# Optimization experiments

Hardware: AMD Instinct MI355X
Metric: run time of the kernel (lower is better)

## Reference

```python
import jax, jax.numpy as jnp
import numpy as np

B = 262144
N_DIM = 8
N_SPLIT = 4
DEPTH = 8
WIDTH = 32
ALPHA = 0.6
LOGSCALE_FACTOR = 3.0


def setup_inputs() -> dict:
    key = jax.random.key(0)
    ks = jax.random.split(key, 8)
    n_out = (N_DIM - N_SPLIT) * 2  # 8
    inp = {
        "x": jax.random.normal(ks[0], (B, N_DIM), dtype=jnp.float32),
        "logdet": jnp.zeros((B, 1), dtype=jnp.float32),
        # actnorm params (stacked over depth)
        "b": jnp.zeros((DEPTH, 1, N_DIM), dtype=jnp.float32),
        "logs": jnp.zeros((DEPTH, 1, N_DIM), dtype=jnp.float32),
        # affine coupling params
        "log_gamma": jnp.zeros((DEPTH, 1, N_DIM - N_SPLIT), dtype=jnp.float32),
        "W1": jax.random.normal(ks[1], (DEPTH, N_SPLIT, WIDTH), dtype=jnp.float32) / np.sqrt(N_SPLIT),
        "b1": jnp.zeros((DEPTH, WIDTH), dtype=jnp.float32),
        "W2": jax.random.normal(ks[2], (DEPTH, WIDTH, WIDTH), dtype=jnp.float32) / np.sqrt(WIDTH),
        "b2": jnp.zeros((DEPTH, WIDTH), dtype=jnp.float32),
        "Wf": jax.random.normal(ks[3], (DEPTH, WIDTH, n_out), dtype=jnp.float32) / np.sqrt(WIDTH),
        "bf": jnp.zeros((DEPTH, n_out), dtype=jnp.float32),
    }
    return inp


def _flow_forward(x, logdet, b, logs, log_gamma, W1, b1, W2, b2, Wf, bf):
    z = x
    ld = logdet
    for i in range(DEPTH):
        # ---- actnorm (with data-dependent init, detached as in torch) ----
        m = jnp.mean(z, axis=0, keepdims=True)
        v = jnp.mean(jnp.square(z - m), axis=0, keepdims=True)
        b_init = jax.lax.stop_gradient(-m)
        logs_init = jax.lax.stop_gradient(
            jnp.log(1.0 / (jnp.sqrt(v) + 1e-6)) / LOGSCALE_FACTOR)
        s = jnp.clip(logs[i] + logs_init, -5.0, 5.0)
        z = (z + (b[i] + b_init)) * jnp.exp(s)
        ld = ld + jnp.sum(s)
        # ---- affine coupling ----
        z1 = z[:, :N_SPLIT]
        z2 = z[:, N_SPLIT:]
        h = jax.nn.relu(z1 @ W1[i] + b1[i])
        h = jax.nn.relu(h @ W2[i] + b2[i])
        h = h @ Wf[i] + bf[i]                      # [B, 2*(n_dim-ns)]
        shift = h[:, 0::2]
        scale = ALPHA * jnp.tanh(h[:, 1::2])
        shift = jnp.exp(jnp.clip(log_gamma[i], -5.0, 5.0)) * jnp.tanh(shift)
        z2 = z2 + scale * z2 + shift
        ld = ld + jnp.sum(jnp.log1p(scale), axis=1, keepdims=True)
        z = jnp.concatenate([z1, z2], axis=1)
        # ---- flip ----
        z = z[:, ::-1]
    return z, ld


def reference(x, logdet, b, logs, log_gamma, W1, b1, W2, b2, Wf, bf):
    return _flow_forward(x, logdet, b, logs, log_gamma, W1, b1, W2, b2, Wf, bf)
```

## Files before the change

### kernel.cpp

```cpp
#include <hip/hip_runtime.h>

#define B_ROWS 262144
#define TPB 1024
#define NBLK 256
#define NGRP 64
#define PADW 32

#define SLOT_L_DW (16 * 64)
#define SLOTS_TOT (9 * SLOT_L_DW)
#define STATS_L_DW 32
#define STATS_TOT (9 * STATS_L_DW)

#define GF_OFF   (NGRP * PADW)
#define BAR_DWORDS (2 * NGRP * PADW)

typedef _Float16 f16;
typedef __attribute__((ext_vector_type(2))) __fp16 fp16x2_t;
typedef __attribute__((ext_vector_type(8))) _Float16 f16x8;
typedef __attribute__((ext_vector_type(4))) float f32x4;
typedef __attribute__((ext_vector_type(16))) float f32x16;
typedef __attribute__((ext_vector_type(2))) unsigned u32x2;

__device__ __forceinline__ float fast_tanh(float x) {
    float e = __expf(2.0f * x);
    return 1.0f - 2.0f * __builtin_amdgcn_rcpf(e + 1.0f);
}
__device__ __forceinline__ float pkh(float a, float b) {
    fp16x2_t h = __builtin_amdgcn_cvt_pkrtz(a, b);
    return __builtin_bit_cast(float, h);
}
__device__ __forceinline__ f16x8 mk8(float a, float b, float c, float d) {
    f32x4 v = {a, b, c, d};
    return __builtin_bit_cast(f16x8, v);
}
__device__ __forceinline__ float bcf(unsigned u) { return __builtin_bit_cast(float, u); }
__device__ __forceinline__ u32x2 pls(float a, float b) {
    return __builtin_amdgcn_permlane32_swap(
        __builtin_bit_cast(unsigned, a), __builtin_bit_cast(unsigned, b),
        false, false);
}

__device__ __forceinline__ void gbar_stats(
    float* slots, float* stats, unsigned* bar, unsigned target, int Lx,
    const float* logs, const float* bvec, const float* lgam, float* lred)
{
    const int tid  = threadIdx.x;
    const int lane = tid & 63;
    const int wid  = tid >> 6;
    const int bid  = blockIdx.x;
    __syncthreads();
    if (wid == 0) {
        if (lane == 0)
            __hip_atomic_fetch_add(bar + (bid >> 2) * PADW, 1u,
                                   __ATOMIC_ACQ_REL, __HIP_MEMORY_SCOPE_AGENT);
        if (bid == 0) {
            const unsigned t4 = target * (NBLK / NGRP);
            while (true) {
                unsigned c = __hip_atomic_load(bar + lane * PADW, __ATOMIC_RELAXED,
                                               __HIP_MEMORY_SCOPE_AGENT);
                if (__all(c >= t4)) break;
                __builtin_amdgcn_s_sleep(1);
            }
            __threadfence();
            const float* sl = slots + (size_t)Lx * SLOT_L_DW;
            float a16[16];
            #pragma unroll
            for (int j = 0; j < 16; ++j)
                a16[j] = __hip_atomic_load(sl + j * 64 + lane, __ATOMIC_RELAXED,
                                           __HIP_MEMORY_SCOPE_AGENT);
            #pragma unroll
            for (int d = 1; d < 64; d <<= 1) {
                #pragma unroll
                for (int j = 0; j < 16; ++j) a16[j] += __shfl_xor(a16[j], d, 64);
            }
            const float invB = 1.0f / (float)B_ROWS;
            float lv0 = 0.f, lv1 = 0.f, sl8 = 0.f, gf = 0.f;
            if (lane < 8) {
                float m = a16[lane] * invB;
                float q = a16[8 + lane] * invB;
                float v = q - m * m;
                v = v < 0.f ? 0.f : v;
                float li = -(1.0f / 3.0f) * __logf(sqrtf(v) + 1e-6f);
                float s = logs[Lx * 8 + lane] + li;
                s = s < -5.f ? -5.f : (s > 5.f ? 5.f : s);
                lv0 = __expf(s);
                lv1 = bvec[Lx * 8 + lane] - m;
                sl8 = s;
            } else if (lane < 12) {
                float lg = lgam[Lx * 4 + (lane - 8)];
                lg = lg < -5.f ? -5.f : (lg > 5.f ? 5.f : lg);
                gf = __expf(lg);
            }
            float ss = sl8;
            ss += __shfl_xor(ss, 1, 64);
            ss += __shfl_xor(ss, 2, 64);
            ss += __shfl_xor(ss, 4, 64);
            float* st = stats + (size_t)Lx * STATS_L_DW;
            if (lane < 8) {
                __hip_atomic_store(st + lane, lv0, __ATOMIC_RELAXED,
                                   __HIP_MEMORY_SCOPE_AGENT);
                __hip_atomic_store(st + 8 + lane, lv1, __ATOMIC_RELAXED,
                                   __HIP_MEMORY_SCOPE_AGENT);
                lred[lane] = lv0; lred[8 + lane] = lv1;
            } else if (lane < 12) {
                __hip_atomic_store(st + 8 + lane, gf, __ATOMIC_RELAXED,
                                   __HIP_MEMORY_SCOPE_AGENT);
                lred[8 + lane] = gf;
            }
            if (lane == 0) {
                __hip_atomic_store(st + 20, ss, __ATOMIC_RELAXED,
                                   __HIP_MEMORY_SCOPE_AGENT);
                lred[20] = ss;
            }
            __hip_atomic_store(bar + GF_OFF + lane * PADW, target,
                               __ATOMIC_RELEASE, __HIP_MEMORY_SCOPE_AGENT);
        } else {
            unsigned* gfp = bar + GF_OFF + (bid >> 2) * PADW;
            while (__hip_atomic_load(gfp, __ATOMIC_RELAXED,
                                     __HIP_MEMORY_SCOPE_AGENT) < target)
                __builtin_amdgcn_s_sleep(1);
            (void)__hip_atomic_load(gfp, __ATOMIC_ACQUIRE,
                                    __HIP_MEMORY_SCOPE_AGENT);
            if (lane < 21)
                lred[lane] = __hip_atomic_load(stats + (size_t)Lx * STATS_L_DW + lane,
                                               __ATOMIC_RELAXED,
                                               __HIP_MEMORY_SCOPE_AGENT);
        }
    }
    __syncthreads();
}

#define PKBLK 80
__global__ void __launch_bounds__(256)
pack_weights(const float* __restrict__ W1, const float* __restrict__ W2,
             const float* __restrict__ Wf,
             f16* __restrict__ w1pk, f16* __restrict__ w2pk, f16* __restrict__ wfpk,
             float* __restrict__ slots, unsigned* __restrict__ bar)
{
    int i = blockIdx.x * 256 + threadIdx.x;
    if (i < 16384) {
        int which = i >> 13;
        int t  = i & 8191;
        int j  = t & 7;
        int ln = (t >> 3) & 63;
        int kh = (t >> 9) & 1;
        int L  = t >> 10;
        int k  = kh * 16 + ((ln >> 5) << 3) + j;
        if (which == 0) {
            w2pk[t] = (f16)W2[L * 1024 + k * 32 + (ln & 31)];
        } else {
            int row = ln & 31;
            wfpk[t] = (row < 8) ? (f16)Wf[L * 256 + k * 8 + row] : (f16)0.f;
        }
    } else {
        int t  = i - 16384;
        int j  = t & 7;
        int ln = (t >> 3) & 63;
        int L  = t >> 9;
        int k  = ((ln >> 5) << 3) + j;
        w1pk[t] = (k < 4) ? (f16)W1[L * 128 + k * 32 + (ln & 31)] : (f16)0.f;
    }
    if (i < SLOTS_TOT) slots[i] = 0.f;
    if (i < BAR_DWORDS) bar[i] = 0u;
}

__global__ void __launch_bounds__(TPB, 4)
flow_fused(const float* __restrict__ x,    const float* __restrict__ logdet,
           const float* __restrict__ bvec, const float* __restrict__ logs,
           const float* __restrict__ log_gamma,
           const float* __restrict__ b1,   const float* __restrict__ b2,
           const float* __restrict__ bf,
           const f16* __restrict__ w1pk,   const f16* __restrict__ w2pk,
           const f16* __restrict__ wfpk,
           float* __restrict__ out,
           float* slots, float* stats, unsigned* __restrict__ bar)
{
    const int tid  = threadIdx.x;
    const int bid  = blockIdx.x;
    const int lane = tid & 63;
    const int wid  = tid >> 6;
    const bool lo  = lane < 32;
    const int slot = bid & 63;
    const int br = ((lane & 1) << 3) | ((lane & 2) << 1) | ((lane & 4) >> 1) | ((lane & 8) >> 3);
    const size_t r0 = (size_t)bid * TPB + tid;

    __shared__ float lred[16 * 16];

    float z[8];
    {
        const float4* p0 = reinterpret_cast<const float4*>(x + r0 * 8);
        float4 a = p0[0], c = p0[1];
        z[0]=a.x; z[1]=a.y; z[2]=a.z; z[3]=a.w;
        z[4]=c.x; z[5]=c.y; z[6]=c.z; z[7]=c.w;
    }
    float ldv = logdet[r0];

    {
        float acc[16];
        #pragma unroll
        for (int j = 0; j < 8; ++j) { acc[j] = z[j]; acc[8 + j] = z[j] * z[j]; }
        #pragma unroll
        for (int i = 0; i < 8; ++i) {
            float snd = (lane & 1) ? acc[i] : acc[8 + i];
            float kp  = (lane & 1) ? acc[8 + i] : acc[i];
            acc[i] = kp + __shfl_xor(snd, 1, 64);
        }
        #pragma unroll
        for (int i = 0; i < 4; ++i) {
            float snd = (lane & 2) ? acc[i] : acc[4 + i];
            float kp  = (lane & 2) ? acc[4 + i] : acc[i];
            acc[i] = kp + __shfl_xor(snd, 2, 64);
        }
        #pragma unroll
        for (int i = 0; i < 2; ++i) {
            float snd = (lane & 4) ? acc[i] : acc[2 + i];
            float kp  = (lane & 4) ? acc[2 + i] : acc[i];
            acc[i] = kp + __shfl_xor(snd, 4, 64);
        }
        {
            float snd = (lane & 8) ? acc[0] : acc[1];
            float kp  = (lane & 8) ? acc[1] : acc[0];
            acc[0] = kp + __shfl_xor(snd, 8, 64);
        }
        acc[0] += __shfl_xor(acc[0], 16, 64);
        acc[0] += __shfl_xor(acc[0], 32, 64);
        if (lane < 16) lred[wid * 16 + br] = acc[0];
        __syncthreads();
        if (tid < 16) {
            float s = 0.f;
            #pragma unroll
            for (int w = 0; w < 16; ++w) s += lred[w * 16 + tid];
            __hip_atomic_fetch_add(slots + tid * 64 + slot, s,
                                   __ATOMIC_RELAXED, __HIP_MEMORY_SCOPE_AGENT);
        }
    }
    gbar_stats(slots, stats, bar, 1, 0, logs, bvec, log_gamma, lred);

    const f16x8* w1p = reinterpret_cast<const f16x8*>(w1pk);
    const f16x8* w2p = reinterpret_cast<const f16x8*>(w2pk);
    const f16x8* wfp = reinterpret_cast<const f16x8*>(wfpk);

    #pragma unroll 1
    for (int L = 0; L < 8; ++L) {
        const f16x8 W1A = w1p[L * 64 + lane];
        const f16x8 A0  = w2p[(L * 2 + 0) * 64 + lane];
        const f16x8 A1  = w2p[(L * 2 + 1) * 64 + lane];
        const f16x8 F0  = wfp[(L * 2 + 0) * 64 + lane];
        const f16x8 F1  = wfp[(L * 2 + 1) * 64 + lane];

        float es[8], beta[8], gfac[4], sum_s;
        #pragma unroll
        for (int j = 0; j < 8; ++j) { es[j] = lred[j]; beta[j] = lred[8 + j]; }
        #pragma unroll
        for (int j = 0; j < 4; ++j) gfac[j] = lred[16 + j];
        sum_s = lred[20];
        __syncthreads();

        #pragma unroll
        for (int j = 0; j < 8; ++j)
            z[j] = (z[j] + beta[j]) * es[j];

        const float* vb1 = b1 + L * 32;
        const float* vb2 = b2 + L * 32;
        const float* vbf = bf + L * 8;

        float zp0 = pkh(z[0], z[1]);
        float zp1 = pkh(z[2], z[3]);
        u32x2 s0 = pls(zp0, 0.f);
        u32x2 s1 = pls(zp1, 0.f);
        f16x8 Z0 = mk8(bcf(s0[0]), bcf(s1[0]), 0.f, 0.f);
        f16x8 Z1 = mk8(bcf(s0[1]), bcf(s1[1]), 0.f, 0.f);

        f32x16 g0 = {}, g1 = {};
        g0 = __builtin_amdgcn_mfma_f32_32x32x16_f16(W1A, Z0, g0, 0, 0, 0);
        g1 = __builtin_amdgcn_mfma_f32_32x32x16_f16(W1A, Z1, g1, 0, 0, 0);

        float qg0[8], qg1[8];
        {
            float h0[16], h1v[16];
            #pragma unroll
            for (int r = 0; r < 16; ++r) {
                int wlo = (r & 3) + 8 * (r >> 2);
                float bsel = lo ? vb1[wlo] : vb1[wlo + 4];
                float a = g0[r] + bsel; h0[r]  = a > 0.f ? a : 0.f;
                float b = g1[r] + bsel; h1v[r] = b > 0.f ? b : 0.f;
            }
            #pragma unroll
            for (int c = 0; c < 8; ++c) {
                qg0[c] = pkh(h0[2 * c], h0[2 * c + 1]);
                qg1[c] = pkh(h1v[2 * c], h1v[2 * c + 1]);
            }
        }

        u32x2 pA = pls(qg0[0], qg0[2]);
        u32x2 pB = pls(qg0[1], qg0[3]);
        u32x2 pC = pls(qg0[4], qg0[6]);
        u32x2 pD = pls(qg0[5], qg0[7]);
        f16x8 B00 = mk8(bcf(pA[0]), bcf(pB[0]), bcf(pA[1]), bcf(pB[1]));
        f16x8 B01 = mk8(bcf(pC[0]), bcf(pD[0]), bcf(pC[1]), bcf(pD[1]));
        pA = pls(qg1[0], qg1[2]);
        pB = pls(qg1[1], qg1[3]);
        pC = pls(qg1[4], qg1[6]);
        pD = pls(qg1[5], qg1[7]);
        f16x8 B10 = mk8(bcf(pA[0]), bcf(pB[0]), bcf(pA[1]), bcf(pB[1]));
        f16x8 B11 = mk8(bcf(pC[0]), bcf(pD[0]), bcf(pC[1]), bcf(pD[1]));

        f32x16 d0 = {}, d1 = {};
        d0 = __builtin_amdgcn_mfma_f32_32x32x16_f16(A0, B00, d0, 0, 0, 0);
        d0 = __builtin_amdgcn_mfma_f32_32x32x16_f16(A1, B01, d0, 0, 0, 0);
        d1 = __builtin_amdgcn_mfma_f32_32x32x16_f16(A0, B10, d1, 0, 0, 0);
        d1 = __builtin_amdgcn_mfma_f32_32x32x16_f16(A1, B11, d1, 0, 0, 0);

        float P0[8], P1[8];
        {
            float h2g0[16], h2g1[16];
            #pragma unroll
            for (int r = 0; r < 16; ++r) {
                int wlo = (r & 3) + 8 * (r >> 2);
                float bsel = lo ? vb2[wlo] : vb2[wlo + 4];
                float a = d0[r] + bsel; h2g0[r] = a > 0.f ? a : 0.f;
                float b = d1[r] + bsel; h2g1[r] = b > 0.f ? b : 0.f;
            }
            #pragma unroll
            for (int c = 0; c < 8; ++c) {
                P0[c] = pkh(h2g0[2 * c], h2g0[2 * c + 1]);
                P1[c] = pkh(h2g1[2 * c], h2g1[2 * c + 1]);
            }
        }

        u32x2 pE = pls(P0[0], P0[2]);
        u32x2 pF = pls(P0[1], P0[3]);
        u32x2 pG = pls(P0[4], P0[6]);
        u32x2 pH = pls(P0[5], P0[7]);
        f16x8 C00 = mk8(bcf(pE[0]), bcf(pF[0]), bcf(pE[1]), bcf(pF[1]));
        f16x8 C01 = mk8(bcf(pG[0]), bcf(pH[0]), bcf(pG[1]), bcf(pH[1]));
        pE = pls(P1[0], P1[2]);
        pF = pls(P1[1], P1[3]);
        pG = pls(P1[4], P1[6]);
        pH = pls(P1[5], P1[7]);
        f16x8 C10 = mk8(bcf(pE[0]), bcf(pF[0]), bcf(pE[1]), bcf(pF[1]));
        f16x8 C11 = mk8(bcf(pG[0]), bcf(pH[0]), bcf(pG[1]), bcf(pH[1]));

        f32x16 e0 = {}, e1 = {};
        e0 = __builtin_amdgcn_mfma_f32_32x32x16_f16(F0, C00, e0, 0, 0, 0);
        e0 = __builtin_amdgcn_mfma_f32_32x32x16_f16(F1, C01, e0, 0, 0, 0);
        e1 = __builtin_amdgcn_mfma_f32_32x32x16_f16(F0, C10, e1, 0, 0, 0);
        e1 = __builtin_amdgcn_mfma_f32_32x32x16_f16(F1, C11, e1, 0, 0, 0);

        float h3[8];
        #pragma unroll
        for (int r = 0; r < 4; ++r) {
            u32x2 pe = pls(e0[r], e1[r]);
            h3[r]     = bcf(pe[0]) + vbf[r];
            h3[r + 4] = bcf(pe[1]) + vbf[r + 4];
        }

        float nacc[16];
        {
            float ldl = 0.f;
            float nz[8];
            #pragma unroll
            for (int j = 0; j < 4; ++j) {
                float sc = 0.6f * fast_tanh(h3[2 * j + 1]);
                float sh = gfac[j] * fast_tanh(h3[2 * j]);
                float z2 = z[4 + j];
                z2 = z2 + sc * z2 + sh;
                ldl += __logf(1.0f + sc);
                nz[3 - j] = z2;
                nz[7 - j] = z[j];
            }
            ldv += sum_s + ldl;
            #pragma unroll
            for (int j = 0; j < 8; ++j) {
                z[j] = nz[j];
                nacc[j]     = nz[j];
                nacc[8 + j] = nz[j] * nz[j];
            }
        }

        if (L < 7) {
            #pragma unroll
            for (int i = 0; i < 8; ++i) {
                float snd = (lane & 1) ? nacc[i] : nacc[8 + i];
                float kp  = (lane & 1) ? nacc[8 + i] : nacc[i];
                nacc[i] = kp + __shfl_xor(snd, 1, 64);
            }
            #pragma unroll
            for (int i = 0; i < 4; ++i) {
                float snd = (lane & 2) ? nacc[i] : nacc[4 + i];
                float kp  = (lane & 2) ? nacc[4 + i] : nacc[i];
                nacc[i] = kp + __shfl_xor(snd, 2, 64);
            }
            #pragma unroll
            for (int i = 0; i < 2; ++i) {
                float snd = (lane & 4) ? nacc[i] : nacc[2 + i];
                float kp  = (lane & 4) ? nacc[2 + i] : nacc[i];
                nacc[i] = kp + __shfl_xor(snd, 4, 64);
            }
            {
                float snd = (lane & 8) ? nacc[0] : nacc[1];
                float kp  = (lane & 8) ? nacc[1] : nacc[0];
                nacc[0] = kp + __shfl_xor(snd, 8, 64);
            }
            nacc[0] += __shfl_xor(nacc[0], 16, 64);
            nacc[0] += __shfl_xor(nacc[0], 32, 64);
            if (lane < 16) lred[wid * 16 + br] = nacc[0];
            __syncthreads();
            if (tid < 16) {
                float s = 0.f;
                #pragma unroll
                for (int w = 0; w < 16; ++w) s += lred[w * 16 + tid];
                __hip_atomic_fetch_add(slots + (size_t)(L + 1) * SLOT_L_DW +
                                           tid * 64 + slot, s,
                                       __ATOMIC_RELAXED, __HIP_MEMORY_SCOPE_AGENT);
            }
            gbar_stats(slots, stats, bar, (unsigned)(L + 2), L + 1,
                       logs, bvec, log_gamma, lred);
        }
    }

    {
        float4* p0 = reinterpret_cast<float4*>(out + r0 * 8);
        float4 a, c;
        a.x=z[0]; a.y=z[1]; a.z=z[2]; a.w=z[3];
        c.x=z[4]; c.y=z[5]; c.z=z[6]; c.w=z[7];
        p0[0] = a; p0[1] = c;
    }
    out[(size_t)B_ROWS * 8 + r0] = ldv;
}

extern "C" void kernel_launch(void* const* d_in, const int* in_sizes, int n_in,
                              void* d_out, int out_size, void* d_ws, size_t ws_size,
                              hipStream_t stream) {
    const float* x      = (const float*)d_in[0];
    const float* logdet = (const float*)d_in[1];
    const float* bvec   = (const float*)d_in[2];
    const float* logs   = (const float*)d_in[3];
    const float* lg     = (const float*)d_in[4];
    const float* W1     = (const float*)d_in[5];
    const float* b1     = (const float*)d_in[6];
    const float* W2     = (const float*)d_in[7];
    const float* b2     = (const float*)d_in[8];
    const float* Wf     = (const float*)d_in[9];
    const float* bf     = (const float*)d_in[10];
    float* out = (float*)d_out;

    f16*      w1pk  = (f16*)d_ws;
    f16*      w2pk  = w1pk + 4096;
    f16*      wfpk  = w2pk + 8192;
    float*    slots = (float*)(wfpk + 8192);
    float*    stats = slots + SLOTS_TOT;
    unsigned* bar   = (unsigned*)(stats + STATS_TOT);

    pack_weights<<<PKBLK, 256, 0, stream>>>(W1, W2, Wf, w1pk, w2pk, wfpk,
                                            slots, bar);

    void* args[] = {&x, &logdet, &bvec, &logs, &lg, &b1, &b2, &bf,
                    &w1pk, &w2pk, &wfpk, &out, &slots, &stats, &bar};
    hipLaunchKernel(reinterpret_cast<void*>(&flow_fused),
                    dim3(NBLK), dim3(TPB), args, 0, stream);
}
```

Baseline: 104.3 us.

## Move global stats reduction to a dedicated coordinator block with per-group broadcast lines

```diff
diff --git a/kernel.cpp b/kernel.cpp
--- a/kernel.cpp
+++ b/kernel.cpp
@@ -2,17 +2,17 @@
 
 #define B_ROWS 262144
 #define TPB 1024
-#define NBLK 256
+#define NROWBLK 256
+#define NBLK 257
 #define NGRP 64
 #define PADW 32
 
 #define SLOT_L_DW (16 * 64)
 #define SLOTS_TOT (9 * SLOT_L_DW)
-#define STATS_L_DW 32
-#define STATS_TOT (9 * STATS_L_DW)
-
-#define GF_OFF   (NGRP * PADW)
-#define BAR_DWORDS (2 * NGRP * PADW)
+#define FL_L_DW (NGRP * PADW)
+#define FL_TOT  (9 * FL_L_DW)
+#define GCNT_DW (NGRP * PADW)
+#define ZERO_DWORDS (SLOTS_TOT + FL_TOT + GCNT_DW)
 
 typedef _Float16 f16;
 typedef __attribute__((ext_vector_type(2))) __fp16 fp16x2_t;
@@ -40,9 +40,8 @@
         false, false);
 }
 
-__device__ __forceinline__ void gbar_stats(
-    float* slots, float* stats, unsigned* bar, unsigned target, int Lx,
-    const float* logs, const float* bvec, const float* lgam, float* lred)
+__device__ __forceinline__ void row_wait(
+    float* fl, unsigned* gcnt, unsigned target, int Lx, float* lred)
 {
     const int tid  = threadIdx.x;
     const int lane = tid & 63;
@@ -51,81 +50,17 @@
     __syncthreads();
     if (wid == 0) {
         if (lane == 0)
-            __hip_atomic_fetch_add(bar + (bid >> 2) * PADW, 1u,
+            __hip_atomic_fetch_add(gcnt + (bid >> 2) * PADW, 1u,
                                    __ATOMIC_ACQ_REL, __HIP_MEMORY_SCOPE_AGENT);
-        if (bid == 0) {
-            const unsigned t4 = target * (NBLK / NGRP);
-            while (true) {
-                unsigned c = __hip_atomic_load(bar + lane * PADW, __ATOMIC_RELAXED,
-                                               __HIP_MEMORY_SCOPE_AGENT);
-                if (__all(c >= t4)) break;
-                __builtin_amdgcn_s_sleep(1);
-            }
-            __threadfence();
-            const float* sl = slots + (size_t)Lx * SLOT_L_DW;
-            float a16[16];
-            #pragma unroll
-            for (int j = 0; j < 16; ++j)
-                a16[j] = __hip_atomic_load(sl + j * 64 + lane, __ATOMIC_RELAXED,
+        const float* line = fl + ((size_t)Lx * NGRP + (bid >> 2)) * PADW;
+        const unsigned* genp = reinterpret_cast<const unsigned*>(line) + 21;
+        while (__hip_atomic_load(genp, __ATOMIC_RELAXED,
+                                 __HIP_MEMORY_SCOPE_AGENT) < target)
+            __builtin_amdgcn_s_sleep(1);
+        (void)__hip_atomic_load(genp, __ATOMIC_ACQUIRE, __HIP_MEMORY_SCOPE_AGENT);
+        if (lane < 21)
+            lred[lane] = __hip_atomic_load(line + lane, __ATOMIC_RELAXED,
                                            __HIP_MEMORY_SCOPE_AGENT);
-            #pragma unroll
-            for (int d = 1; d < 64; d <<= 1) {
-                #pragma unroll
-                for (int j = 0; j < 16; ++j) a16[j] += __shfl_xor(a16[j], d, 64);
-            }
-            const float invB = 1.0f / (float)B_ROWS;
-            float lv0 = 0.f, lv1 = 0.f, sl8 = 0.f, gf = 0.f;
-            if (lane < 8) {
-                float m = a16[lane] * invB;
-                float q = a16[8 + lane] * invB;
-                float v = q - m * m;
-                v = v < 0.f ? 0.f : v;
-                float li = -(1.0f / 3.0f) * __logf(sqrtf(v) + 1e-6f);
-                float s = logs[Lx * 8 + lane] + li;
-                s = s < -5.f ? -5.f : (s > 5.f ? 5.f : s);
-                lv0 = __expf(s);
-                lv1 = bvec[Lx * 8 + lane] - m;
-                sl8 = s;
-            } else if (lane < 12) {
-                float lg = lgam[Lx * 4 + (lane - 8)];
-                lg = lg < -5.f ? -5.f : (lg > 5.f ? 5.f : lg);
-                gf = __expf(lg);
-            }
-            float ss = sl8;
-            ss += __shfl_xor(ss, 1, 64);
-            ss += __shfl_xor(ss, 2, 64);
-            ss += __shfl_xor(ss, 4, 64);
-            float* st = stats + (size_t)Lx * STATS_L_DW;
-            if (lane < 8) {
-                __hip_atomic_store(st + lane, lv0, __ATOMIC_RELAXED,
-                                   __HIP_MEMORY_SCOPE_AGENT);
-                __hip_atomic_store(st + 8 + lane, lv1, __ATOMIC_RELAXED,
-                                   __HIP_MEMORY_SCOPE_AGENT);
-                lred[lane] = lv0; lred[8 + lane] = lv1;
-            } else if (lane < 12) {
-                __hip_atomic_store(st + 8 + lane, gf, __ATOMIC_RELAXED,
-                                   __HIP_MEMORY_SCOPE_AGENT);
-                lred[8 + lane] = gf;
-            }
-            if (lane == 0) {
-                __hip_atomic_store(st + 20, ss, __ATOMIC_RELAXED,
-                                   __HIP_MEMORY_SCOPE_AGENT);
-                lred[20] = ss;
-            }
-            __hip_atomic_store(bar + GF_OFF + lane * PADW, target,
-                               __ATOMIC_RELEASE, __HIP_MEMORY_SCOPE_AGENT);
-        } else {
-            unsigned* gfp = bar + GF_OFF + (bid >> 2) * PADW;
-            while (__hip_atomic_load(gfp, __ATOMIC_RELAXED,
-                                     __HIP_MEMORY_SCOPE_AGENT) < target)
-                __builtin_amdgcn_s_sleep(1);
-            (void)__hip_atomic_load(gfp, __ATOMIC_ACQUIRE,
-                                    __HIP_MEMORY_SCOPE_AGENT);
-            if (lane < 21)
-                lred[lane] = __hip_atomic_load(stats + (size_t)Lx * STATS_L_DW + lane,
-                                               __ATOMIC_RELAXED,
-                                               __HIP_MEMORY_SCOPE_AGENT);
-        }
     }
     __syncthreads();
 }
@@ -135,7 +70,7 @@
 pack_weights(const float* __restrict__ W1, const float* __restrict__ W2,
              const float* __restrict__ Wf,
              f16* __restrict__ w1pk, f16* __restrict__ w2pk, f16* __restrict__ wfpk,
-             float* __restrict__ slots, unsigned* __restrict__ bar)
+             float* __restrict__ zbase)
 {
     int i = blockIdx.x * 256 + threadIdx.x;
     if (i < 16384) {
@@ -160,11 +95,11 @@
         int k  = ((ln >> 5) << 3) + j;
         w1pk[t] = (k < 4) ? (f16)W1[L * 128 + k * 32 + (ln & 31)] : (f16)0.f;
     }
-    if (i < SLOTS_TOT) slots[i] = 0.f;
-    if (i < BAR_DWORDS) bar[i] = 0u;
-}
-
-__global__ void __launch_bounds__(TPB, 4)
+    for (int t = i; t < ZERO_DWORDS; t += PKBLK * 256)
+        zbase[t] = 0.f;
+}
+
+__global__ void __launch_bounds__(TPB, 8)
 flow_fused(const float* __restrict__ x,    const float* __restrict__ logdet,
            const float* __restrict__ bvec, const float* __restrict__ logs,
            const float* __restrict__ log_gamma,
@@ -173,12 +108,82 @@
            const f16* __restrict__ w1pk,   const f16* __restrict__ w2pk,
            const f16* __restrict__ wfpk,
            float* __restrict__ out,
-           float* slots, float* stats, unsigned* __restrict__ bar)
+           float* slots, float* fl, unsigned* __restrict__ gcnt)
 {
     const int tid  = threadIdx.x;
     const int bid  = blockIdx.x;
     const int lane = tid & 63;
     const int wid  = tid >> 6;
+
+    if (bid == NROWBLK) {
+        if (wid == 0) {
+            #pragma unroll 1
+            for (int t = 1; t <= 8; ++t) {
+                const int Lx = t - 1;
+                const unsigned t4 = (unsigned)(4 * t);
+                while (true) {
+                    unsigned c = __hip_atomic_load(gcnt + lane * PADW,
+                                                   __ATOMIC_RELAXED,
+                                                   __HIP_MEMORY_SCOPE_AGENT);
+                    if (__all(c >= t4)) break;
+                    __builtin_amdgcn_s_sleep(1);
+                }
+                __threadfence();
+                const float* sl = slots + (size_t)Lx * SLOT_L_DW;
+                float a16[16];
+                #pragma unroll
+                for (int j = 0; j < 16; ++j)
+                    a16[j] = __hip_atomic_load(sl + j * 64 + lane,
+                                               __ATOMIC_RELAXED,
+                                               __HIP_MEMORY_SCOPE_AGENT);
+                #pragma unroll
+                for (int d = 1; d < 64; d <<= 1) {
+                    #pragma unroll
+                    for (int j = 0; j < 16; ++j) a16[j] += __shfl_xor(a16[j], d, 64);
+                }
+                const float invB = 1.0f / (float)B_ROWS;
+                float lv0 = 0.f, lv1 = 0.f, sl8 = 0.f, gf = 0.f;
+                if (lane < 8) {
+                    float m = a16[lane] * invB;
+                    float q = a16[8 + lane] * invB;
+                    float v = q - m * m;
+                    v = v < 0.f ? 0.f : v;
+                    float li = -(1.0f / 3.0f) * __logf(sqrtf(v) + 1e-6f);
+                    float s = logs[Lx * 8 + lane] + li;
+                    s = s < -5.f ? -5.f : (s > 5.f ? 5.f : s);
+                    lv0 = __expf(s);
+                    lv1 = bvec[Lx * 8 + lane] - m;
+                    sl8 = s;
+                } else if (lane < 12) {
+                    float lg = log_gamma[Lx * 4 + (lane - 8)];
+                    lg = lg < -5.f ? -5.f : (lg > 5.f ? 5.f : lg);
+                    gf = __expf(lg);
+                }
+                float ss = sl8;
+                ss += __shfl_xor(ss, 1, 64);
+                ss += __shfl_xor(ss, 2, 64);
+                ss += __shfl_xor(ss, 4, 64);
+                float stv[21];
+                #pragma unroll
+                for (int j = 0; j < 8; ++j) stv[j]      = __shfl(lv0, j, 64);
+                #pragma unroll
+                for (int j = 0; j < 8; ++j) stv[8 + j]  = __shfl(lv1, j, 64);
+                #pragma unroll
+                for (int j = 0; j < 4; ++j) stv[16 + j] = __shfl(gf, 8 + j, 64);
+                stv[20] = __shfl(ss, 0, 64);
+                float* line = fl + ((size_t)Lx * NGRP + lane) * PADW;
+                #pragma unroll
+                for (int j = 0; j < 21; ++j)
+                    __hip_atomic_store(line + j, stv[j], __ATOMIC_RELAXED,
+                                       __HIP_MEMORY_SCOPE_AGENT);
+                __hip_atomic_store(reinterpret_cast<unsigned*>(line) + 21,
+                                   (unsigned)t, __ATOMIC_RELEASE,
+                                   __HIP_MEMORY_SCOPE_AGENT);
+            }
+        }
+        return;
+    }
+
     const bool lo  = lane < 32;
     const int slot = bid & 63;
     const int br = ((lane & 1) << 3) | ((lane & 2) << 1) | ((lane & 4) >> 1) | ((lane & 8) >> 3);
@@ -234,7 +239,7 @@
                                    __ATOMIC_RELAXED, __HIP_MEMORY_SCOPE_AGENT);
         }
     }
-    gbar_stats(slots, stats, bar, 1, 0, logs, bvec, log_gamma, lred);
+    row_wait(fl, gcnt, 1, 0, lred);
 
     const f16x8* w1p = reinterpret_cast<const f16x8*>(w1pk);
     const f16x8* w2p = reinterpret_cast<const f16x8*>(w2pk);
@@ -414,8 +419,7 @@
                                            tid * 64 + slot, s,
                                        __ATOMIC_RELAXED, __HIP_MEMORY_SCOPE_AGENT);
             }
-            gbar_stats(slots, stats, bar, (unsigned)(L + 2), L + 1,
-                       logs, bvec, log_gamma, lred);
+            row_wait(fl, gcnt, (unsigned)(L + 2), L + 1, lred);
         }
     }
 
@@ -449,14 +453,13 @@
     f16*      w2pk  = w1pk + 4096;
     f16*      wfpk  = w2pk + 8192;
     float*    slots = (float*)(wfpk + 8192);
-    float*    stats = slots + SLOTS_TOT;
-    unsigned* bar   = (unsigned*)(stats + STATS_TOT);
-
-    pack_weights<<<PKBLK, 256, 0, stream>>>(W1, W2, Wf, w1pk, w2pk, wfpk,
-                                            slots, bar);
+    float*    fl    = slots + SLOTS_TOT;
+    unsigned* gcnt  = (unsigned*)(fl + FL_TOT);
+
+    pack_weights<<<PKBLK, 256, 0, stream>>>(W1, W2, Wf, w1pk, w2pk, wfpk, slots);
 
     void* args[] = {&x, &logdet, &bvec, &logs, &lg, &b1, &b2, &bf,
-                    &w1pk, &w2pk, &wfpk, &out, &slots, &stats, &bar};
+                    &w1pk, &w2pk, &wfpk, &out, &slots, &fl, &gcnt};
     hipLaunchKernel(reinterpret_cast<void*>(&flow_fused),
                     dim3(NBLK), dim3(TPB), args, 0, stream);
 }
```

Result: slower. 221.3 us (+112.2%).
